# Kernel optimization log

Hardware: AMD Instinct MI355X
Metric: run time of the kernel (lower is better)

## Reference

```python
import jax, jax.numpy as jnp
import numpy as np

D, H, DH, L, DFF, V, K = 512, 8, 64, 6, 2048, 256, 5
N = 10240
TAU = 0.1
EPS = 1e-5


def _ln(x, w, b):
    m = x.mean(-1, keepdims=True)
    v = ((x - m) ** 2).mean(-1, keepdims=True)
    return (x - m) * jax.lax.rsqrt(v + EPS) * w + b


def _attn(q_in, kv_in, inw, inb, ow, ob):
    # q_in: [Q, D], kv_in: [M, D]; standard PyTorch MultiheadAttention math
    wq, wk, wv = jnp.split(inw, 3, 0)
    bq, bk, bv = jnp.split(inb, 3)
    q = (q_in @ wq.T + bq).reshape(-1, H, DH)
    k = (kv_in @ wk.T + bk).reshape(-1, H, DH)
    v = (kv_in @ wv.T + bv).reshape(-1, H, DH)
    s = jnp.einsum('qhd,mhd->hqm', q, k) / np.float32(np.sqrt(DH))
    o = jnp.einsum('hqm,mhd->qhd', jax.nn.softmax(s, -1), v).reshape(-1, D)
    return o @ ow.T + ob


def setup_inputs() -> dict:
    key = jax.random.key(0)
    ks = iter(jax.random.split(key, 64))

    def w(shape):
        return jax.random.normal(next(ks), shape, jnp.float32) * 0.02

    inp = {
        'input_bytes': jax.random.randint(next(ks), (N,), 0, V, jnp.int32),
        'emb': w((V, D)),
        'alpha': jnp.float32(0.5),
        'enc_inw': w((L, 3 * D, D)), 'enc_inb': w((L, 3 * D)),
        'enc_ow': w((L, D, D)), 'enc_ob': w((L, D)),
        'enc_w1': w((L, DFF, D)), 'enc_b1': w((L, DFF)),
        'enc_w2': w((L, D, DFF)), 'enc_b2': w((L, D)),
        'enc_ln1w': jnp.ones((L, D)), 'enc_ln1b': jnp.zeros((L, D)),
        'enc_ln2w': jnp.ones((L, D)), 'enc_ln2b': jnp.zeros((L, D)),
        'dec_sa_inw': w((L, 3 * D, D)), 'dec_sa_inb': w((L, 3 * D)),
        'dec_sa_ow': w((L, D, D)), 'dec_sa_ob': w((L, D)),
        'dec_ca_inw': w((L, 3 * D, D)), 'dec_ca_inb': w((L, 3 * D)),
        'dec_ca_ow': w((L, D, D)), 'dec_ca_ob': w((L, D)),
        'dec_w1': w((L, DFF, D)), 'dec_b1': w((L, DFF)),
        'dec_w2': w((L, D, DFF)), 'dec_b2': w((L, D)),
        'dec_ln1w': jnp.ones((L, D)), 'dec_ln1b': jnp.zeros((L, D)),
        'dec_ln2w': jnp.ones((L, D)), 'dec_ln2b': jnp.zeros((L, D)),
        'dec_ln3w': jnp.ones((L, D)), 'dec_ln3b': jnp.zeros((L, D)),
        'out_w': w((V, D)), 'out_b': w((V,)),
    }
    return inp


def reference(input_bytes, emb, alpha, enc_inw, enc_inb, enc_ow, enc_ob,
              enc_w1, enc_b1, enc_w2, enc_b2, enc_ln1w, enc_ln1b, enc_ln2w, enc_ln2b,
              dec_sa_inw, dec_sa_inb, dec_sa_ow, dec_sa_ob,
              dec_ca_inw, dec_ca_inb, dec_ca_ow, dec_ca_ob,
              dec_w1, dec_b1, dec_w2, dec_b2,
              dec_ln1w, dec_ln1b, dec_ln2w, dec_ln2b, dec_ln3w, dec_ln3b,
              out_w, out_b):
    P = input_bytes.shape[0] // K
    patches = input_bytes[:P * K].reshape(P, K)            # fixed k-byte patching
    x = emb[patches].mean(1)                               # mean-pooled patch embeddings [P, D]
    # ---- TransformerEncoder (post-LN, relu FFN, no dropout at eval) ----
    for l in range(L):
        x = _ln(x + _attn(x, x, enc_inw[l], enc_inb[l], enc_ow[l], enc_ob[l]), enc_ln1w[l], enc_ln1b[l])
        ff = jax.nn.relu(x @ enc_w1[l].T + enc_b1[l]) @ enc_w2[l].T + enc_b2[l]
        x = _ln(x + ff, enc_ln2w[l], enc_ln2b[l])
    encoded = x                                            # [P, D]
    # ---- gating + embedding mix (vectorized over the per-patch loop) ----
    gate = jnp.linalg.norm(encoded, axis=-1) > TAU
    tok = emb[patches[:, -1]]
    x = jnp.where(gate[:, None], alpha * encoded + (1.0 - alpha) * tok, tok)  # [P, D]
    # ---- TransformerDecoder: each patch is an independent length-1 target;
    #      self-attn over a single token reduces to out_proj(V(x));
    #      cross-attn attends to the full encoded memory (as in the original loop) ----
    for l in range(L):
        wv = dec_sa_inw[l][2 * D:]
        bv = dec_sa_inb[l][2 * D:]
        sa = (x @ wv.T + bv) @ dec_sa_ow[l].T + dec_sa_ob[l]
        x = _ln(x + sa, dec_ln1w[l], dec_ln1b[l])
        ca = _attn(x, encoded, dec_ca_inw[l], dec_ca_inb[l], dec_ca_ow[l], dec_ca_ob[l])
        x = _ln(x + ca, dec_ln2w[l], dec_ln2b[l])
        ff = jax.nn.relu(x @ dec_w1[l].T + dec_b1[l]) @ dec_w2[l].T + dec_b2[l]
        x = _ln(x + ff, dec_ln3w[l], dec_ln3b[l])
    return x @ out_w.T + out_b                             # [P, V]
```

## Files before the change

### kernel.cpp

```cpp
#include <hip/hip_runtime.h>
#include <hip/hip_bf16.h>
#include <math.h>

#define DD   512
#define HN   8
#define DHD  64
#define LL   6
#define DFF_ 2048
#define VV   256
#define KB_  5
#define PP   2048
#define EPS_ 1e-5f
#define TAU_ 0.1f
#define NS   4
#define KVS  (PP / NS)

typedef __attribute__((ext_vector_type(8))) short bf16x8;
typedef __attribute__((ext_vector_type(4))) short bf16x4;
typedef __attribute__((ext_vector_type(4))) float f32x4;

__device__ __forceinline__ float wave_sum(float v) {
#pragma unroll
  for (int m = 32; m >= 1; m >>= 1) v += __shfl_xor(v, m, 64);
  return v;
}

__device__ __forceinline__ unsigned short f2bf(float f) {
  unsigned u = __float_as_uint(f);
  u += 0x7FFF + ((u >> 16) & 1);
  return (unsigned short)(u >> 16);
}

__device__ __forceinline__ float bf2f(unsigned short u) {
  return __uint_as_float(((unsigned)u) << 16);
}

__device__ __forceinline__ bf16x8 cvt8(float4 a, float4 b) {
  bf16x8 v;
  v[0] = (short)f2bf(a.x); v[1] = (short)f2bf(a.y);
  v[2] = (short)f2bf(a.z); v[3] = (short)f2bf(a.w);
  v[4] = (short)f2bf(b.x); v[5] = (short)f2bf(b.y);
  v[6] = (short)f2bf(b.z); v[7] = (short)f2bf(b.w);
  return v;
}

__device__ __forceinline__ void gload16(const void* g, void* l) {
  __builtin_amdgcn_global_load_lds(
      (const __attribute__((address_space(1))) unsigned int*)g,
      (__attribute__((address_space(3))) unsigned int*)l, 16, 0, 0);
}

#define NSEG 55
struct CvtSeg { const float* src; short* dst; int n; };
struct CvtArgs { CvtSeg seg[NSEG]; };

__global__ __launch_bounds__(256) void convert_bf16_kernel(CvtArgs a) {
  const CvtSeg sg = a.seg[blockIdx.y];
  const int i = ((int)blockIdx.x * 256 + (int)threadIdx.x) * 16;
  if (i >= sg.n) return;
  const float4 x0 = *(const float4*)(sg.src + i);
  const float4 x1 = *(const float4*)(sg.src + i + 4);
  const float4 x2 = *(const float4*)(sg.src + i + 8);
  const float4 x3 = *(const float4*)(sg.src + i + 12);
  *(bf16x8*)(sg.dst + i)     = cvt8(x0, x1);
  *(bf16x8*)(sg.dst + i + 8) = cvt8(x2, x3);
}

__global__ __launch_bounds__(256) void transpose_wv_kernel(const float* __restrict__ sa_inw,
                                                           short* __restrict__ wvt) {
  __shared__ float t[64][65];
  const int l = blockIdx.z;
  const float* S = sa_inw + (size_t)l * 3 * DD * DD + (size_t)2 * DD * DD;
  short* D = wvt + (size_t)l * DD * DD;
  const int bo = blockIdx.y * 64;
  const int bi = blockIdx.x * 64;
  const int r = (int)threadIdx.x >> 2;
  const int c0 = ((int)threadIdx.x & 3) * 16;
#pragma unroll
  for (int j = 0; j < 16; j += 4)
    *(float4*)&t[r][c0 + j] = *(const float4*)&S[(size_t)(bo + r) * DD + bi + c0 + j];
  __syncthreads();
  bf16x8 o0, o1;
#pragma unroll
  for (int j = 0; j < 8; ++j) o0[j] = (short)f2bf(t[c0 + j][r]);
#pragma unroll
  for (int j = 0; j < 8; ++j) o1[j] = (short)f2bf(t[c0 + 8 + j][r]);
  short* dp = &D[(size_t)(bi + r) * DD + bo + c0];
  *(bf16x8*)dp = o0;
  *(bf16x8*)(dp + 8) = o1;
}

__global__ __launch_bounds__(256) void sa_bias_kernel(const float* __restrict__ sa_inb,
                                                      const float* __restrict__ sa_ow,
                                                      const float* __restrict__ sa_ob,
                                                      float* __restrict__ bc) {
  const int gid = (int)blockIdx.x * 4 + ((int)threadIdx.x >> 6);
  const int l = gid >> 9, n = gid & 511;
  const int lane = (int)threadIdx.x & 63;
  const float* wo = sa_ow + (size_t)l * DD * DD + (size_t)n * DD + lane * 8;
  const float* bv = sa_inb + (size_t)l * 3 * DD + 2 * DD + lane * 8;
  float s = 0.f;
#pragma unroll
  for (int j = 0; j < 8; ++j) s += wo[j] * bv[j];
  s = wave_sum(s);
  if (lane == 0) bc[(size_t)l * DD + n] = s + sa_ob[(size_t)l * DD + n];
}

__global__ __launch_bounds__(256) void gemm_wc_kernel(const short* __restrict__ WoBase,
                                                      size_t astr,
                                                      const short* __restrict__ WvT,
                                                      short* __restrict__ Wc) {
  constexpr int BK = 64;
  __shared__ short As[64 * BK];
  __shared__ short Bs[64 * BK];
  const int l = blockIdx.z;
  const short* A = WoBase + (size_t)l * astr;
  const short* W = WvT + (size_t)l * DD * DD;
  short* C = Wc + (size_t)l * DD * DD;
  const int tid = (int)threadIdx.x;
  const int lane = tid & 63;
  const int wid = tid >> 6;
  const int wm = (wid >> 1) * 32;
  const int wn = (wid & 1) * 32;
  const int bm = blockIdx.y * 64;
  const int bn = blockIdx.x * 64;
  const int fr = lane & 15;
  const int kq = lane >> 4;
  const int rs = fr & 7;
  const int srow = lane >> 3;
  const int scg = (lane & 7) ^ srow;

  f32x4 acc[2][2];
#pragma unroll
  for (int i = 0; i < 2; ++i)
#pragma unroll
    for (int j = 0; j < 2; ++j) acc[i][j] = (f32x4){0.f, 0.f, 0.f, 0.f};

  for (int k0 = 0; k0 < DD; k0 += BK) {
    __syncthreads();
#pragma unroll
    for (int is = 0; is < 2; ++is) {
      const int ib = is * 4 + wid;
      gload16(&A[(size_t)(bm + ib * 8 + srow) * DD + k0 + scg * 8], &As[ib * 512]);
      gload16(&W[(size_t)(bn + ib * 8 + srow) * DD + k0 + scg * 8], &Bs[ib * 512]);
    }
    __syncthreads();
#pragma unroll
    for (int s = 0; s < 2; ++s) {
      const int cg = s * 4 + kq;
      const int co = (cg ^ rs) * 8;
      bf16x8 af[2], bf[2];
#pragma unroll
      for (int i = 0; i < 2; ++i) af[i] = *(const bf16x8*)&As[(wm + i * 16 + fr) * BK + co];
#pragma unroll
      for (int j = 0; j < 2; ++j) bf[j] = *(const bf16x8*)&Bs[(wn + j * 16 + fr) * BK + co];
#pragma unroll
      for (int i = 0; i < 2; ++i)
#pragma unroll
        for (int j = 0; j < 2; ++j)
          acc[i][j] = __builtin_amdgcn_mfma_f32_16x16x32_bf16(af[i], bf[j], acc[i][j], 0, 0, 0);
    }
  }
  const int cr = (lane >> 4) * 4;
#pragma unroll
  for (int j = 0; j < 2; ++j) {
    const int col = bn + wn + j * 16 + fr;
#pragma unroll
    for (int i = 0; i < 2; ++i)
#pragma unroll
      for (int r = 0; r < 4; ++r)
        C[(size_t)(bm + wm + i * 16 + cr + r) * DD + col] = (short)f2bf(acc[i][j][r]);
  }
}

__global__ __launch_bounds__(256) void embed_mean_kernel(const int* __restrict__ bytes,
                                                         const float* __restrict__ emb,
                                                         float* __restrict__ x,
                                                         short* __restrict__ xb,
                                                         float* __restrict__ tok) {
  const int p = blockIdx.x;
  const int d = threadIdx.x * 2;
  float a0 = 0.f, a1 = 0.f;
  int last = 0;
#pragma unroll
  for (int k = 0; k < KB_; ++k) {
    const int idx = bytes[p * KB_ + k];
    last = idx;
    const float* e = emb + (size_t)idx * DD + d;
    a0 += e[0]; a1 += e[1];
  }
  a0 *= 0.2f; a1 *= 0.2f;
  x[(size_t)p * DD + d]     = a0;
  x[(size_t)p * DD + d + 1] = a1;
  xb[(size_t)p * DD + d]     = (short)f2bf(a0);
  xb[(size_t)p * DD + d + 1] = (short)f2bf(a1);
  const float* e = emb + (size_t)last * DD + d;
  tok[(size_t)p * DD + d]     = e[0];
  tok[(size_t)p * DD + d + 1] = e[1];
}

template <int BM, int BN, int NSPLIT, int RELU, int WF32, int WBF16, int QS>
__global__ __launch_bounds__(256) void gemm_gl_kernel(
    const short* __restrict__ A, int lda,
    const short* __restrict__ W, int ldw,
    const float* __restrict__ bias,
    float* __restrict__ Cf, short* __restrict__ Cb, int ldc, int Kd,
    size_t pstride) {
  constexpr int BK = 128;
  __shared__ short As[BM * BK];
  __shared__ short Bs[BN * BK];
  constexpr int WM = BM / 2, WN = BN / 2;
  constexpr int MF = WM / 16, NF = WN / 16;
  const int tid = (int)threadIdx.x;
  const int lane = tid & 63;
  const int wid = tid >> 6;
  const int wm = (wid >> 1) * WM;
  const int wn = (wid & 1) * WN;
  const int bm = blockIdx.y * BM;
  const int bn = blockIdx.x * BN;
  const int fr = lane & 15;
  const int kq = lane >> 4;
  const int srow = lane >> 4;
  const int sc16 = lane & 15;

  const int kz = (NSPLIT > 1) ? (int)blockIdx.z : 0;
  const int kbeg = kz * (Kd / NSPLIT);
  const int kend = kbeg + Kd / NSPLIT;

  f32x4 acc[MF][NF];
#pragma unroll
  for (int i = 0; i < MF; ++i)
#pragma unroll
    for (int j = 0; j < NF; ++j) acc[i][j] = (f32x4){0.f, 0.f, 0.f, 0.f};

  for (int k0 = kbeg; k0 < kend; k0 += BK) {
    __syncthreads();
#pragma unroll
    for (int is = 0; is < BM / 16; ++is) {
      const int ib = is * 4 + wid;
      const int row = ib * 4 + srow;
      const int cg = sc16 ^ (row & 15);
      gload16(&A[(size_t)(bm + row) * lda + k0 + cg * 8], &As[ib * 512]);
    }
#pragma unroll
    for (int is = 0; is < BN / 16; ++is) {
      const int ib = is * 4 + wid;
      const int row = ib * 4 + srow;
      const int cg = sc16 ^ (row & 15);
      gload16(&W[(size_t)(bn + row) * ldw + k0 + cg * 8], &Bs[ib * 512]);
    }
    __syncthreads();
#pragma unroll
    for (int s = 0; s < 4; ++s) {
      const int co = ((s * 4 + kq) ^ fr) * 8;
      bf16x8 af[MF], bf[NF];
#pragma unroll
      for (int i = 0; i < MF; ++i)
        af[i] = *(const bf16x8*)&As[(wm + i * 16 + fr) * BK + co];
#pragma unroll
      for (int j = 0; j < NF; ++j)
        bf[j] = *(const bf16x8*)&Bs[(wn + j * 16 + fr) * BK + co];
#pragma unroll
      for (int i = 0; i < MF; ++i)
#pragma unroll
        for (int j = 0; j < NF; ++j)
          acc[i][j] = __builtin_amdgcn_mfma_f32_16x16x32_bf16(af[i], bf[j], acc[i][j], 0, 0, 0);
    }
  }

  const int cr = (lane >> 4) * 4;
  if constexpr (NSPLIT > 1) {
#pragma unroll
    for (int j = 0; j < NF; ++j) {
      const int col = bn + wn + j * 16 + fr;
#pragma unroll
      for (int i = 0; i < MF; ++i)
#pragma unroll
        for (int r = 0; r < 4; ++r) {
          const size_t idx = (size_t)(bm + wm + i * 16 + cr + r) * ldc + col;
          if (WF32) Cf[(size_t)kz * pstride + idx] = acc[i][j][r];
          else      Cb[(size_t)kz * pstride + idx] = (short)f2bf(acc[i][j][r]);
        }
    }
  } else {
#pragma unroll
    for (int j = 0; j < NF; ++j) {
      const int col = bn + wn + j * 16 + fr;
      const float bb = bias[col];
      const float sc = (QS && col < DD) ? 0.125f : 1.f;
#pragma unroll
      for (int i = 0; i < MF; ++i) {
#pragma unroll
        for (int r = 0; r < 4; ++r) {
          float v = (acc[i][j][r] + bb) * sc;
          if (RELU) v = fmaxf(v, 0.f);
          const size_t idx = (size_t)(bm + wm + i * 16 + cr + r) * ldc + col;
          if (WF32) Cf[idx] = v;
          if (WBF16) Cb[idx] = (short)f2bf(v);
        }
      }
    }
  }
}

__global__ __launch_bounds__(256) void gemm_ca_kernel(
    const short* __restrict__ Aq, const short* __restrict__ Akv,
    const short* __restrict__ Wfull, const float* __restrict__ bias,
    short* __restrict__ Cb) {
  constexpr int BK = 64;
  __shared__ short As[64 * BK];
  __shared__ short Bs[64 * BK];
  const int bx = (int)blockIdx.x;
  const int part_kv = bx >= 8;
  const short* A = part_kv ? Akv : Aq;
  const int wrow0 = part_kv ? DD + (bx - 8) * 64 : bx * 64;
  const float sc = part_kv ? 1.f : 0.125f;
  const int tid = (int)threadIdx.x;
  const int lane = tid & 63;
  const int wid = tid >> 6;
  const int wm = (wid >> 1) * 32;
  const int wn = (wid & 1) * 32;
  const int bm = blockIdx.y * 64;
  const int fr = lane & 15;
  const int kq = lane >> 4;
  const int rs = fr & 7;
  const int srow = lane >> 3;
  const int scg = (lane & 7) ^ srow;

  f32x4 acc[2][2];
#pragma unroll
  for (int i = 0; i < 2; ++i)
#pragma unroll
    for (int j = 0; j < 2; ++j) acc[i][j] = (f32x4){0.f, 0.f, 0.f, 0.f};

  for (int k0 = 0; k0 < DD; k0 += BK) {
    __syncthreads();
#pragma unroll
    for (int is = 0; is < 2; ++is) {
      const int ib = is * 4 + wid;
      gload16(&A[(size_t)(bm + ib * 8 + srow) * DD + k0 + scg * 8], &As[ib * 512]);
      gload16(&Wfull[(size_t)(wrow0 + ib * 8 + srow) * DD + k0 + scg * 8], &Bs[ib * 512]);
    }
    __syncthreads();
#pragma unroll
    for (int s = 0; s < 2; ++s) {
      const int cg = s * 4 + kq;
      const int co = (cg ^ rs) * 8;
      bf16x8 af[2], bf[2];
#pragma unroll
      for (int i = 0; i < 2; ++i) af[i] = *(const bf16x8*)&As[(wm + i * 16 + fr) * BK + co];
#pragma unroll
      for (int j = 0; j < 2; ++j) bf[j] = *(const bf16x8*)&Bs[(wn + j * 16 + fr) * BK + co];
#pragma unroll
      for (int i = 0; i < 2; ++i)
#pragma unroll
        for (int j = 0; j < 2; ++j)
          acc[i][j] = __builtin_amdgcn_mfma_f32_16x16x32_bf16(af[i], bf[j], acc[i][j], 0, 0, 0);
    }
  }
  const int cr = (lane >> 4) * 4;
#pragma unroll
  for (int j = 0; j < 2; ++j) {
    const int col = wrow0 + wn + j * 16 + fr;
    const float bb = bias[col];
#pragma unroll
    for (int i = 0; i < 2; ++i)
#pragma unroll
      for (int r = 0; r < 4; ++r)
        Cb[(size_t)(bm + wm + i * 16 + cr + r) * (3 * DD) + col] =
            (short)f2bf((acc[i][j][r] + bb) * sc);
  }
}

__global__ __launch_bounds__(256) void flash_attn_mfma_kernel(const short* __restrict__ qkvb,
                                                              short* __restrict__ Opart,
                                                              float* __restrict__ stats) {
  constexpr int LS = 72;
  __shared__ short Ks[64 * 64];
  __shared__ short Vt[64 * LS];
  __shared__ short Ps[64 * LS];
  const int h = blockIdx.y;
  const int q0 = blockIdx.x * 64;
  const int sp = blockIdx.z;
  const int tid = (int)threadIdx.x;
  const int lane = tid & 63;
  const int wid = tid >> 6;
  const int fr = lane & 15;
  const int g = lane >> 4;
  const int kg = g * 8;
  const int rs3 = fr & 7;

  bf16x8 qf[2];
  {
    const short* src = qkvb + (size_t)(q0 + wid * 16 + fr) * (3 * DD) + h * DHD + kg;
    qf[0] = *(const bf16x8*)src;
    qf[1] = *(const bf16x8*)(src + 32);
  }

  f32x4 acc_o[4];
#pragma unroll
  for (int df = 0; df < 4; ++df) acc_o[df] = (f32x4){0.f, 0.f, 0.f, 0.f};
  float mreg = -INFINITY, lsum = 0.f;

  const int srow8 = lane >> 3;
  const int sscg = (lane & 7) ^ srow8;
  const int vk2 = (tid & 31) * 2;
  const int vd8 = (tid >> 5) * 8;

  for (int t = 0; t < KVS / 64; ++t) {
    const int k0 = sp * KVS + t * 64;
    __syncthreads();
    {
#pragma unroll
      for (int p = 0; p < 2; ++p) {
        const int rb = p * 32 + wid * 8;
        gload16(&qkvb[(size_t)(k0 + rb + srow8) * (3 * DD) + DD + h * DHD + sscg * 8],
                &Ks[rb * 64]);
      }
      const short* vbase = qkvb + (size_t)(k0 + vk2) * (3 * DD) + 2 * DD + h * DHD + vd8;
      const bf16x8 v0 = *(const bf16x8*)vbase;
      const bf16x8 v1 = *(const bf16x8*)(vbase + 3 * DD);
#pragma unroll
      for (int j = 0; j < 8; ++j) {
        const unsigned pk = ((unsigned)(unsigned short)v0[j]) |
                            (((unsigned)(unsigned short)v1[j]) << 16);
        *(unsigned*)&Vt[(vd8 + j) * LS + vk2] = pk;
      }
    }
    __syncthreads();

    f32x4 st[4];
#pragma unroll
    for (int nf = 0; nf < 4; ++nf) st[nf] = (f32x4){0.f, 0.f, 0.f, 0.f};
    __builtin_amdgcn_s_setprio(1);
#pragma unroll
    for (int nf = 0; nf < 4; ++nf) {
      const int krow = (nf * 16 + fr) * 64;
      const bf16x8 kf0 = *(const bf16x8*)&Ks[krow + ((g ^ rs3) * 8)];
      const bf16x8 kf1 = *(const bf16x8*)&Ks[krow + (((g + 4) ^ rs3) * 8)];
      st[nf] = __builtin_amdgcn_mfma_f32_16x16x32_bf16(kf0, qf[0], st[nf], 0, 0, 0);
      st[nf] = __builtin_amdgcn_mfma_f32_16x16x32_bf16(kf1, qf[1], st[nf], 0, 0, 0);
    }
    __builtin_amdgcn_s_setprio(0);

    float mx = st[0][0];
#pragma unroll
    for (int nf = 0; nf < 4; ++nf)
#pragma unroll
      for (int i = 0; i < 4; ++i) mx = fmaxf(mx, st[nf][i]);
    mx = fmaxf(mx, __shfl_xor(mx, 16, 64));
    mx = fmaxf(mx, __shfl_xor(mx, 32, 64));
    const float mn = fmaxf(mreg, mx);
    const float corr = __expf(mreg - mn);
    mreg = mn;
    float pv[4][4];
    float sum = 0.f;
#pragma unroll
    for (int nf = 0; nf < 4; ++nf)
#pragma unroll
      for (int i = 0; i < 4; ++i) {
        pv[nf][i] = __expf(st[nf][i] - mn);
        sum += pv[nf][i];
      }
    sum += __shfl_xor(sum, 16, 64);
    sum += __shfl_xor(sum, 32, 64);
    lsum = lsum * corr + sum;

    float corr_acc[4];
#pragma unroll
    for (int i = 0; i < 4; ++i)
      corr_acc[i] = __shfl(corr, (lane & 48) | (g * 4 + i), 64);
#pragma unroll
    for (int df = 0; df < 4; ++df) {
      acc_o[df][0] *= corr_acc[0]; acc_o[df][1] *= corr_acc[1];
      acc_o[df][2] *= corr_acc[2]; acc_o[df][3] *= corr_acc[3];
    }

#pragma unroll
    for (int nf = 0; nf < 4; ++nf) {
      bf16x4 pw;
#pragma unroll
      for (int i = 0; i < 4; ++i) pw[i] = (short)f2bf(pv[nf][i]);
      *(bf16x4*)&Ps[(wid * 16 + fr) * LS + nf * 16 + g * 4] = pw;
    }
    asm volatile("s_waitcnt lgkmcnt(0)" ::: "memory");

    const bf16x8 pa0 = *(const bf16x8*)&Ps[(wid * 16 + fr) * LS + kg];
    const bf16x8 pa1 = *(const bf16x8*)&Ps[(wid * 16 + fr) * LS + kg + 32];
    __builtin_amdgcn_s_setprio(1);
#pragma unroll
    for (int df = 0; df < 4; ++df) {
      const bf16x8 vb0 = *(const bf16x8*)&Vt[(df * 16 + fr) * LS + kg];
      const bf16x8 vb1 = *(const bf16x8*)&Vt[(df * 16 + fr) * LS + kg + 32];
      acc_o[df] = __builtin_amdgcn_mfma_f32_16x16x32_bf16(pa0, vb0, acc_o[df], 0, 0, 0);
      acc_o[df] = __builtin_amdgcn_mfma_f32_16x16x32_bf16(pa1, vb1, acc_o[df], 0, 0, 0);
    }
    __builtin_amdgcn_s_setprio(0);
  }

  const int orow = q0 + wid * 16 + g * 4;
#pragma unroll
  for (int df = 0; df < 4; ++df)
#pragma unroll
    for (int i = 0; i < 4; ++i)
      Opart[((size_t)sp * PP + orow + i) * DD + h * DHD + df * 16 + fr] =
          (short)f2bf(acc_o[df][i]);
  if (g == 0) {
    const size_t si = (((size_t)sp * PP + q0 + wid * 16 + fr) * HN + h) * 2;
    stats[si]     = mreg;
    stats[si + 1] = lsum;
  }
}

__global__ __launch_bounds__(256) void attn_combine_kernel(const short* __restrict__ Opart,
                                                           const float* __restrict__ stats,
                                                           short* __restrict__ outb) {
  const int row = blockIdx.x * 4 + ((int)threadIdx.x >> 6);
  const int lane = (int)threadIdx.x & 63;
  const int d0 = lane * 8;
  const int h = d0 >> 6;
  float m[NS], l[NS];
  float M = -INFINITY;
#pragma unroll
  for (int s = 0; s < NS; ++s) {
    const size_t si = (((size_t)s * PP + row) * HN + h) * 2;
    m[s] = stats[si]; l[s] = stats[si + 1];
    M = fmaxf(M, m[s]);
  }
  float L = 0.f;
  float o[8];
#pragma unroll
  for (int j = 0; j < 8; ++j) o[j] = 0.f;
#pragma unroll
  for (int s = 0; s < NS; ++s) {
    const float e = __expf(m[s] - M);
    L += l[s] * e;
    const bf16x8 v = *(const bf16x8*)&Opart[((size_t)s * PP + row) * DD + d0];
#pragma unroll
    for (int j = 0; j < 8; ++j) o[j] += bf2f((unsigned short)v[j]) * e;
  }
  const float inv = 1.f / L;
  bf16x8 ob;
#pragma unroll
  for (int j = 0; j < 8; ++j) ob[j] = (short)f2bf(o[j] * inv);
  *(bf16x8*)&outb[(size_t)row * DD + d0] = ob;
}

__global__ __launch_bounds__(256) void ln_residual_kernel(const float* __restrict__ xin,
                                                          const short* __restrict__ pA,
                                                          const short* __restrict__ pB,
                                                          const float* __restrict__ gb,
                                                          const float* __restrict__ w,
                                                          const float* __restrict__ b,
                                                          float* __restrict__ out,
                                                          short* __restrict__ outb) {
  const int row = blockIdx.x * 4 + (threadIdx.x >> 6);
  const int lane = threadIdx.x & 63;
  const size_t base = (size_t)row * DD + lane * 8;
  float v[8];
  {
    const float4 a0 = *(const float4*)&xin[base];
    const float4 a1 = *(const float4*)&xin[base + 4];
    const bf16x8 r = *(const bf16x8*)&pA[base];
    const bf16x8 s = *(const bf16x8*)&pB[base];
    const float4 g0 = *(const float4*)&gb[lane * 8];
    const float4 g1 = *(const float4*)&gb[lane * 8 + 4];
    v[0] = a0.x + bf2f((unsigned short)r[0]) + bf2f((unsigned short)s[0]) + g0.x;
    v[1] = a0.y + bf2f((unsigned short)r[1]) + bf2f((unsigned short)s[1]) + g0.y;
    v[2] = a0.z + bf2f((unsigned short)r[2]) + bf2f((unsigned short)s[2]) + g0.z;
    v[3] = a0.w + bf2f((unsigned short)r[3]) + bf2f((unsigned short)s[3]) + g0.w;
    v[4] = a1.x + bf2f((unsigned short)r[4]) + bf2f((unsigned short)s[4]) + g1.x;
    v[5] = a1.y + bf2f((unsigned short)r[5]) + bf2f((unsigned short)s[5]) + g1.y;
    v[6] = a1.z + bf2f((unsigned short)r[6]) + bf2f((unsigned short)s[6]) + g1.z;
    v[7] = a1.w + bf2f((unsigned short)r[7]) + bf2f((unsigned short)s[7]) + g1.w;
  }
  float sum = 0.f;
#pragma unroll
  for (int j = 0; j < 8; ++j) sum += v[j];
  sum = wave_sum(sum);
  const float mean = sum * (1.f / DD);
  float sq = 0.f;
#pragma unroll
  for (int j = 0; j < 8; ++j) { const float dd = v[j] - mean; sq += dd * dd; }
  sq = wave_sum(sq);
  const float rstd = rsqrtf(sq * (1.f / DD) + EPS_);
  const float* wp = w + lane * 8;
  const float* bp = b + lane * 8;
  float o[8];
#pragma unroll
  for (int j = 0; j < 8; ++j) o[j] = (v[j] - mean) * rstd * wp[j] + bp[j];
  *(float4*)&out[base] = *(float4*)&o[0];
  *(float4*)&out[base + 4] = *(float4*)&o[4];
  bf16x8 ob;
#pragma unroll
  for (int j = 0; j < 8; ++j) ob[j] = (short)f2bf(o[j]);
  *(bf16x8*)&outb[base] = ob;
}

__global__ __launch_bounds__(256) void ln_gate_kernel(const float* __restrict__ xin,
                                                      const short* __restrict__ pA,
                                                      const short* __restrict__ pB,
                                                      const float* __restrict__ gb,
                                                      const float* __restrict__ w,
                                                      const float* __restrict__ b,
                                                      const float* __restrict__ tok,
                                                      const float* __restrict__ alpha_p,
                                                      float* __restrict__ xout,
                                                      short* __restrict__ xb,
                                                      short* __restrict__ encb) {
  const int row = blockIdx.x * 4 + (threadIdx.x >> 6);
  const int lane = threadIdx.x & 63;
  const size_t base = (size_t)row * DD + lane * 8;
  float v[8];
  {
    const float4 a0 = *(const float4*)&xin[base];
    const float4 a1 = *(const float4*)&xin[base + 4];
    const bf16x8 r = *(const bf16x8*)&pA[base];
    const bf16x8 s = *(const bf16x8*)&pB[base];
    const float4 g0 = *(const float4*)&gb[lane * 8];
    const float4 g1 = *(const float4*)&gb[lane * 8 + 4];
    v[0] = a0.x + bf2f((unsigned short)r[0]) + bf2f((unsigned short)s[0]) + g0.x;
    v[1] = a0.y + bf2f((unsigned short)r[1]) + bf2f((unsigned short)s[1]) + g0.y;
    v[2] = a0.z + bf2f((unsigned short)r[2]) + bf2f((unsigned short)s[2]) + g0.z;
    v[3] = a0.w + bf2f((unsigned short)r[3]) + bf2f((unsigned short)s[3]) + g0.w;
    v[4] = a1.x + bf2f((unsigned short)r[4]) + bf2f((unsigned short)s[4]) + g1.x;
    v[5] = a1.y + bf2f((unsigned short)r[5]) + bf2f((unsigned short)s[5]) + g1.y;
    v[6] = a1.z + bf2f((unsigned short)r[6]) + bf2f((unsigned short)s[6]) + g1.z;
    v[7] = a1.w + bf2f((unsigned short)r[7]) + bf2f((unsigned short)s[7]) + g1.w;
  }
  float sum = 0.f;
#pragma unroll
  for (int j = 0; j < 8; ++j) sum += v[j];
  sum = wave_sum(sum);
  const float mean = sum * (1.f / DD);
  float sq = 0.f;
#pragma unroll
  for (int j = 0; j < 8; ++j) { const float dd = v[j] - mean; sq += dd * dd; }
  sq = wave_sum(sq);
  const float rstd = rsqrtf(sq * (1.f / DD) + EPS_);
  const float* wp = w + lane * 8;
  const float* bp = b + lane * 8;
  float e[8];
#pragma unroll
  for (int j = 0; j < 8; ++j) e[j] = (v[j] - mean) * rstd * wp[j] + bp[j];
  bf16x8 eb;
#pragma unroll
  for (int j = 0; j < 8; ++j) eb[j] = (short)f2bf(e[j]);
  *(bf16x8*)&encb[base] = eb;
  float nsq = 0.f;
#pragma unroll
  for (int j = 0; j < 8; ++j) nsq += e[j] * e[j];
  nsq = wave_sum(nsq);
  const bool gate = nsq > TAU_ * TAU_;
  const float a = *alpha_p;
  float t[8];
  {
    const float4 b0 = *(const float4*)&tok[base];
    const float4 b1 = *(const float4*)&tok[base + 4];
    t[0] = b0.x; t[1] = b0.y; t[2] = b0.z; t[3] = b0.w;
    t[4] = b1.x; t[5] = b1.y; t[6] = b1.z; t[7] = b1.w;
  }
  float o[8];
#pragma unroll
  for (int j = 0; j < 8; ++j) o[j] = gate ? (a * e[j] + (1.f - a) * t[j]) : t[j];
  *(float4*)&xout[base] = *(float4*)&o[0];
  *(float4*)&xout[base + 4] = *(float4*)&o[4];
  bf16x8 ob;
#pragma unroll
  for (int j = 0; j < 8; ++j) ob[j] = (short)f2bf(o[j]);
  *(bf16x8*)&xb[base] = ob;
}

__global__ __launch_bounds__(256) void out_combine_kernel(const float* __restrict__ P0,
                                                          const float* __restrict__ P1,
                                                          const float* __restrict__ bias,
                                                          float* __restrict__ out) {
  const size_t i = ((size_t)blockIdx.x * 256 + threadIdx.x) * 4;
  const int col = (int)(i % VV);
  const float4 a = *(const float4*)&P0[i];
  const float4 b = *(const float4*)&P1[i];
  const float4 c = *(const float4*)&bias[col];
  float4 o;
  o.x = a.x + b.x + c.x; o.y = a.y + b.y + c.y;
  o.z = a.z + b.z + c.z; o.w = a.w + b.w + c.w;
  *(float4*)&out[i] = o;
}

extern "C" void kernel_launch(void* const* d_in, const int* in_sizes, int n_in,
                              void* d_out, int out_size, void* d_ws, size_t ws_size,
                              hipStream_t stream) {
  const int*   bytes    = (const int*)d_in[0];
  const float* emb      = (const float*)d_in[1];
  const float* alpha    = (const float*)d_in[2];
  const float* enc_inw  = (const float*)d_in[3];
  const float* enc_inb  = (const float*)d_in[4];
  const float* enc_ow   = (const float*)d_in[5];
  const float* enc_ob   = (const float*)d_in[6];
  const float* enc_w1   = (const float*)d_in[7];
  const float* enc_b1   = (const float*)d_in[8];
  const float* enc_w2   = (const float*)d_in[9];
  const float* enc_b2   = (const float*)d_in[10];
  const float* enc_ln1w = (const float*)d_in[11];
  const float* enc_ln1b = (const float*)d_in[12];
  const float* enc_ln2w = (const float*)d_in[13];
  const float* enc_ln2b = (const float*)d_in[14];
  const float* dec_sa_inw = (const float*)d_in[15];
  const float* dec_sa_inb = (const float*)d_in[16];
  const float* dec_sa_ow  = (const float*)d_in[17];
  const float* dec_sa_ob  = (const float*)d_in[18];
  const float* dec_ca_inw = (const float*)d_in[19];
  const float* dec_ca_inb = (const float*)d_in[20];
  const float* dec_ca_ow  = (const float*)d_in[21];
  const float* dec_ca_ob  = (const float*)d_in[22];
  const float* dec_w1   = (const float*)d_in[23];
  const float* dec_b1   = (const float*)d_in[24];
  const float* dec_w2   = (const float*)d_in[25];
  const float* dec_b2   = (const float*)d_in[26];
  const float* dec_ln1w = (const float*)d_in[27];
  const float* dec_ln1b = (const float*)d_in[28];
  const float* dec_ln2w = (const float*)d_in[29];
  const float* dec_ln2b = (const float*)d_in[30];
  const float* dec_ln3w = (const float*)d_in[31];
  const float* dec_ln3b = (const float*)d_in[32];
  const float* out_w    = (const float*)d_in[33];
  const float* out_b    = (const float*)d_in[34];

  float* fp = (float*)d_ws;
  float* x     = fp;  fp += (size_t)PP * DD;
  float* tok   = fp;  fp += (size_t)PP * DD;
  float* stats = fp;  fp += (size_t)NS * PP * HN * 2;
  float* outP  = fp;  fp += (size_t)2 * PP * VV;
  float* bcbuf = fp;  fp += (size_t)LL * DD;
  short* sp = (short*)fp;
  short* OpartB  = sp;  sp += (size_t)NS * PP * DD;
  short* tmpB    = sp;  sp += (size_t)2 * PP * DD;
  short* x_bf    = sp;  sp += (size_t)PP * DD;
  short* enc_bf  = sp;  sp += (size_t)PP * DD;
  short* qkv_bf  = sp;  sp += (size_t)PP * 3 * DD;
  short* attno_bf= sp;  sp += (size_t)PP * DD;
  short* ffh_bf  = sp;  sp += (size_t)PP * DFF_;
  short* wvT     = sp;  sp += (size_t)LL * DD * DD;
  short* wcM     = sp;  sp += (size_t)LL * DD * DD;
  short* warena  = sp;

  CvtArgs ca;
  size_t eoff[LL][4], doff[LL][5], ooff;
  size_t dec_start = 0, dec_stride = 0;
  {
    int si = 0;
    size_t off = 0;
    const size_t n0 = 3 * DD * DD, n1 = DD * DD, n2 = (size_t)DFF_ * DD, n3 = (size_t)DD * DFF_;
    for (int l = 0; l < LL; ++l) {
      ca.seg[si++] = {enc_inw + (size_t)l * n0, warena + off, (int)n0}; eoff[l][0] = off; off += n0;
      ca.seg[si++] = {enc_ow  + (size_t)l * n1, warena + off, (int)n1}; eoff[l][1] = off; off += n1;
      ca.seg[si++] = {enc_w1  + (size_t)l * n2, warena + off, (int)n2}; eoff[l][2] = off; off += n2;
      ca.seg[si++] = {enc_w2  + (size_t)l * n3, warena + off, (int)n3}; eoff[l][3] = off; off += n3;
    }
    dec_start = off;
    for (int l = 0; l < LL; ++l) {
      const size_t o0 = off;
      ca.seg[si++] = {dec_sa_ow  + (size_t)l * n1, warena + off, (int)n1}; doff[l][0] = off; off += n1;
      ca.seg[si++] = {dec_ca_inw + (size_t)l * n0, warena + off, (int)n0}; doff[l][1] = off; off += n0;
      ca.seg[si++] = {dec_ca_ow  + (size_t)l * n1, warena + off, (int)n1}; doff[l][2] = off; off += n1;
      ca.seg[si++] = {dec_w1     + (size_t)l * n2, warena + off, (int)n2}; doff[l][3] = off; off += n2;
      ca.seg[si++] = {dec_w2     + (size_t)l * n3, warena + off, (int)n3}; doff[l][4] = off; off += n3;
      if (l == 0) dec_stride = off - o0; (void)o0;
    }
    ca.seg[si++] = {out_w, warena + off, VV * DD}; ooff = off;
  }

  const dim3 b256(256);
  const dim3 gFA(PP / 64, HN, NS);
  const dim3 gQKV(3 * DD / 64, PP / 128);
  const dim3 gFF1(DFF_ / 64, PP / 128);
  const dim3 gS(DD / 64, PP / 64, 2);
  const dim3 gCA(24, PP / 64);
  const dim3 gOUTg(VV / 64, PP / 64, 2);
  const size_t psD = (size_t)PP * DD;
  const size_t psV = (size_t)PP * VV;

  convert_bf16_kernel<<<dim3(256, NSEG), b256, 0, stream>>>(ca);
  transpose_wv_kernel<<<dim3(8, 8, LL), b256, 0, stream>>>(dec_sa_inw, wvT);
  sa_bias_kernel<<<(LL * DD) / 4, b256, 0, stream>>>(dec_sa_inb, dec_sa_ow, dec_sa_ob, bcbuf);
  gemm_wc_kernel<<<dim3(8, 8, LL), b256, 0, stream>>>(warena + dec_start, dec_stride, wvT, wcM);
  embed_mean_kernel<<<PP, b256, 0, stream>>>(bytes, emb, x, x_bf, tok);

  for (int l = 0; l < LL; ++l) {
    const float* inb = enc_inb + (size_t)l * 3 * DD;
    const float* ob  = enc_ob  + (size_t)l * DD;
    const float* b1  = enc_b1  + (size_t)l * DFF_;
    const float* b2  = enc_b2  + (size_t)l * DD;

    gemm_gl_kernel<128, 64, 1, 0, 0, 1, 1><<<gQKV, b256, 0, stream>>>(
        x_bf, DD, warena + eoff[l][0], DD, inb, nullptr, qkv_bf, 3 * DD, DD, 0);
    flash_attn_mfma_kernel<<<gFA, b256, 0, stream>>>(qkv_bf, OpartB, stats);
    attn_combine_kernel<<<PP / 4, b256, 0, stream>>>(OpartB, stats, attno_bf);
    gemm_gl_kernel<64, 64, 2, 0, 0, 0, 0><<<gS, b256, 0, stream>>>(
        attno_bf, DD, warena + eoff[l][1], DD, nullptr, nullptr, tmpB, DD, DD, psD);
    ln_residual_kernel<<<PP / 4, b256, 0, stream>>>(
        x, tmpB, tmpB + psD, ob, enc_ln1w + (size_t)l * DD, enc_ln1b + (size_t)l * DD, x, x_bf);
    gemm_gl_kernel<128, 64, 1, 1, 0, 1, 0><<<gFF1, b256, 0, stream>>>(
        x_bf, DD, warena + eoff[l][2], DD, b1, nullptr, ffh_bf, DFF_, DD, 0);
    gemm_gl_kernel<64, 64, 2, 0, 0, 0, 0><<<gS, b256, 0, stream>>>(
        ffh_bf, DFF_, warena + eoff[l][3], DFF_, nullptr, nullptr, tmpB, DD, DFF_, psD);
    if (l + 1 < LL) {
      ln_residual_kernel<<<PP / 4, b256, 0, stream>>>(
          x, tmpB, tmpB + psD, b2, enc_ln2w + (size_t)l * DD, enc_ln2b + (size_t)l * DD, x, x_bf);
    } else {
      ln_gate_kernel<<<PP / 4, b256, 0, stream>>>(
          x, tmpB, tmpB + psD, b2, enc_ln2w + (size_t)l * DD, enc_ln2b + (size_t)l * DD,
          tok, alpha, x, x_bf, enc_bf);
    }
  }

  for (int l = 0; l < LL; ++l) {
    const float* ca_inb = dec_ca_inb + (size_t)l * 3 * DD;
    const float* ca_ob  = dec_ca_ob + (size_t)l * DD;
    const float* b1 = dec_b1 + (size_t)l * DFF_;
    const float* b2 = dec_b2 + (size_t)l * DD;

    gemm_gl_kernel<64, 64, 2, 0, 0, 0, 0><<<gS, b256, 0, stream>>>(
        x_bf, DD, wcM + (size_t)l * DD * DD, DD, nullptr, nullptr, tmpB, DD, DD, psD);
    ln_residual_kernel<<<PP / 4, b256, 0, stream>>>(
        x, tmpB, tmpB + psD, bcbuf + (size_t)l * DD,
        dec_ln1w + (size_t)l * DD, dec_ln1b + (size_t)l * DD, x, x_bf);

    gemm_ca_kernel<<<gCA, b256, 0, stream>>>(
        x_bf, enc_bf, warena + doff[l][1], ca_inb, qkv_bf);
    flash_attn_mfma_kernel<<<gFA, b256, 0, stream>>>(qkv_bf, OpartB, stats);
    attn_combine_kernel<<<PP / 4, b256, 0, stream>>>(OpartB, stats, attno_bf);
    gemm_gl_kernel<64, 64, 2, 0, 0, 0, 0><<<gS, b256, 0, stream>>>(
        attno_bf, DD, warena + doff[l][2], DD, nullptr, nullptr, tmpB, DD, DD, psD);
    ln_residual_kernel<<<PP / 4, b256, 0, stream>>>(
        x, tmpB, tmpB + psD, ca_ob, dec_ln2w + (size_t)l * DD, dec_ln2b + (size_t)l * DD, x, x_bf);

    gemm_gl_kernel<128, 64, 1, 1, 0, 1, 0><<<gFF1, b256, 0, stream>>>(
        x_bf, DD, warena + doff[l][3], DD, b1, nullptr, ffh_bf, DFF_, DD, 0);
    gemm_gl_kernel<64, 64, 2, 0, 0, 0, 0><<<gS, b256, 0, stream>>>(
        ffh_bf, DFF_, warena + doff[l][4], DFF_, nullptr, nullptr, tmpB, DD, DFF_, psD);
    ln_residual_kernel<<<PP / 4, b256, 0, stream>>>(
        x, tmpB, tmpB + psD, b2, dec_ln3w + (size_t)l * DD, dec_ln3b + (size_t)l * DD, x, x_bf);
  }

  gemm_gl_kernel<64, 64, 2, 0, 1, 0, 0><<<gOUTg, b256, 0, stream>>>(
      x_bf, DD, warena + ooff, DD, nullptr, outP, nullptr, VV, DD, psV);
  out_combine_kernel<<<(PP * VV / 4) / 256, b256, 0, stream>>>(
      outP, outP + psV, out_b, (float*)d_out);
}
```

Measured before the change: 989.8 us.

## Drop fp32 residual stream, use exp2 softmax with lazy max rescaling

The fp32 copy of the residual stream is removed, so the layernorm kernels read and write only the bf16 activation buffer. The flash-attention softmax moves to base-2 exponentials by folding log2(e) into the query scale. It also skips the running-max rescale of the accumulators unless the new maximum exceeds the old one by a threshold. This cuts memory traffic in the LN kernels and exp/shuffle work in attention, at the cost of keeping the residual stream only in bf16 across all layers.

After: 981.4 us. About the same (-0.8%).

```diff
diff --git a/kernel.cpp b/kernel.cpp
--- a/kernel.cpp
+++ b/kernel.cpp
@@ -14,6 +14,8 @@
 #define TAU_ 0.1f
 #define NS   4
 #define KVS  (PP / NS)
+#define QSCALE 0.18033688f
+#define THRL2  11.5416f
 
 typedef __attribute__((ext_vector_type(8))) short bf16x8;
 typedef __attribute__((ext_vector_type(4))) short bf16x4;
@@ -175,7 +177,6 @@
 
 __global__ __launch_bounds__(256) void embed_mean_kernel(const int* __restrict__ bytes,
                                                          const float* __restrict__ emb,
-                                                         float* __restrict__ x,
                                                          short* __restrict__ xb,
                                                          float* __restrict__ tok) {
   const int p = blockIdx.x;
@@ -189,11 +190,8 @@
     const float* e = emb + (size_t)idx * DD + d;
     a0 += e[0]; a1 += e[1];
   }
-  a0 *= 0.2f; a1 *= 0.2f;
-  x[(size_t)p * DD + d]     = a0;
-  x[(size_t)p * DD + d + 1] = a1;
-  xb[(size_t)p * DD + d]     = (short)f2bf(a0);
-  xb[(size_t)p * DD + d + 1] = (short)f2bf(a1);
+  xb[(size_t)p * DD + d]     = (short)f2bf(a0 * 0.2f);
+  xb[(size_t)p * DD + d + 1] = (short)f2bf(a1 * 0.2f);
   const float* e = emb + (size_t)last * DD + d;
   tok[(size_t)p * DD + d]     = e[0];
   tok[(size_t)p * DD + d + 1] = e[1];
@@ -287,7 +285,7 @@
     for (int j = 0; j < NF; ++j) {
       const int col = bn + wn + j * 16 + fr;
       const float bb = bias[col];
-      const float sc = (QS && col < DD) ? 0.125f : 1.f;
+      const float sc = (QS && col < DD) ? QSCALE : 1.f;
 #pragma unroll
       for (int i = 0; i < MF; ++i) {
 #pragma unroll
@@ -314,7 +312,7 @@
   const int part_kv = bx >= 8;
   const short* A = part_kv ? Akv : Aq;
   const int wrow0 = part_kv ? DD + (bx - 8) * 64 : bx * 64;
-  const float sc = part_kv ? 1.f : 0.125f;
+  const float sc = part_kv ? 1.f : QSCALE;
   const int tid = (int)threadIdx.x;
   const int lane = tid & 63;
   const int wid = tid >> 6;
@@ -450,31 +448,35 @@
       for (int i = 0; i < 4; ++i) mx = fmaxf(mx, st[nf][i]);
     mx = fmaxf(mx, __shfl_xor(mx, 16, 64));
     mx = fmaxf(mx, __shfl_xor(mx, 32, 64));
-    const float mn = fmaxf(mreg, mx);
-    const float corr = __expf(mreg - mn);
-    mreg = mn;
+
+    if (!__all(mx <= mreg + THRL2)) {
+      const float mn = fmaxf(mreg, mx);
+      const float corr = exp2f(mreg - mn);
+      mreg = mn;
+      lsum *= corr;
+      float corr_acc[4];
+#pragma unroll
+      for (int i = 0; i < 4; ++i)
+        corr_acc[i] = __shfl(corr, (lane & 48) | (g * 4 + i), 64);
+#pragma unroll
+      for (int df = 0; df < 4; ++df) {
+        acc_o[df][0] *= corr_acc[0]; acc_o[df][1] *= corr_acc[1];
+        acc_o[df][2] *= corr_acc[2]; acc_o[df][3] *= corr_acc[3];
+      }
+    }
+
     float pv[4][4];
     float sum = 0.f;
 #pragma unroll
     for (int nf = 0; nf < 4; ++nf)
 #pragma unroll
       for (int i = 0; i < 4; ++i) {
-        pv[nf][i] = __expf(st[nf][i] - mn);
+        pv[nf][i] = exp2f(st[nf][i] - mreg);
         sum += pv[nf][i];
       }
     sum += __shfl_xor(sum, 16, 64);
     sum += __shfl_xor(sum, 32, 64);
-    lsum = lsum * corr + sum;
-
-    float corr_acc[4];
-#pragma unroll
-    for (int i = 0; i < 4; ++i)
-      corr_acc[i] = __shfl(corr, (lane & 48) | (g * 4 + i), 64);
-#pragma unroll
-    for (int df = 0; df < 4; ++df) {
-      acc_o[df][0] *= corr_acc[0]; acc_o[df][1] *= corr_acc[1];
-      acc_o[df][2] *= corr_acc[2]; acc_o[df][3] *= corr_acc[3];
-    }
+    lsum += sum;
 
 #pragma unroll
     for (int nf = 0; nf < 4; ++nf) {
@@ -533,7 +535,7 @@
   for (int j = 0; j < 8; ++j) o[j] = 0.f;
 #pragma unroll
   for (int s = 0; s < NS; ++s) {
-    const float e = __expf(m[s] - M);
+    const float e = exp2f(m[s] - M);
     L += l[s] * e;
     const bf16x8 v = *(const bf16x8*)&Opart[((size_t)s * PP + row) * DD + d0];
 #pragma unroll
@@ -546,33 +548,28 @@
   *(bf16x8*)&outb[(size_t)row * DD + d0] = ob;
 }
 
-__global__ __launch_bounds__(256) void ln_residual_kernel(const float* __restrict__ xin,
+__global__ __launch_bounds__(256) void ln_residual_kernel(const short* __restrict__ xin,
                                                           const short* __restrict__ pA,
                                                           const short* __restrict__ pB,
                                                           const float* __restrict__ gb,
                                                           const float* __restrict__ w,
                                                           const float* __restrict__ b,
-                                                          float* __restrict__ out,
                                                           short* __restrict__ outb) {
   const int row = blockIdx.x * 4 + (threadIdx.x >> 6);
   const int lane = threadIdx.x & 63;
   const size_t base = (size_t)row * DD + lane * 8;
   float v[8];
   {
-    const float4 a0 = *(const float4*)&xin[base];
-    const float4 a1 = *(const float4*)&xin[base + 4];
+    const bf16x8 a = *(const bf16x8*)&xin[base];
     const bf16x8 r = *(const bf16x8*)&pA[base];
     const bf16x8 s = *(const bf16x8*)&pB[base];
     const float4 g0 = *(const float4*)&gb[lane * 8];
     const float4 g1 = *(const float4*)&gb[lane * 8 + 4];
-    v[0] = a0.x + bf2f((unsigned short)r[0]) + bf2f((unsigned short)s[0]) + g0.x;
-    v[1] = a0.y + bf2f((unsigned short)r[1]) + bf2f((unsigned short)s[1]) + g0.y;
-    v[2] = a0.z + bf2f((unsigned short)r[2]) + bf2f((unsigned short)s[2]) + g0.z;
-    v[3] = a0.w + bf2f((unsigned short)r[3]) + bf2f((unsigned short)s[3]) + g0.w;
-    v[4] = a1.x + bf2f((unsigned short)r[4]) + bf2f((unsigned short)s[4]) + g1.x;
-    v[5] = a1.y + bf2f((unsigned short)r[5]) + bf2f((unsigned short)s[5]) + g1.y;
-    v[6] = a1.z + bf2f((unsigned short)r[6]) + bf2f((unsigned short)s[6]) + g1.z;
-    v[7] = a1.w + bf2f((unsigned short)r[7]) + bf2f((unsigned short)s[7]) + g1.w;
+    const float gg[8] = {g0.x, g0.y, g0.z, g0.w, g1.x, g1.y, g1.z, g1.w};
+#pragma unroll
+    for (int j = 0; j < 8; ++j)
+      v[j] = bf2f((unsigned short)a[j]) + bf2f((unsigned short)r[j]) +
+             bf2f((unsigned short)s[j]) + gg[j];
   }
   float sum = 0.f;
 #pragma unroll
@@ -586,18 +583,14 @@
   const float rstd = rsqrtf(sq * (1.f / DD) + EPS_);
   const float* wp = w + lane * 8;
   const float* bp = b + lane * 8;
-  float o[8];
-#pragma unroll
-  for (int j = 0; j < 8; ++j) o[j] = (v[j] - mean) * rstd * wp[j] + bp[j];
-  *(float4*)&out[base] = *(float4*)&o[0];
-  *(float4*)&out[base + 4] = *(float4*)&o[4];
   bf16x8 ob;
 #pragma unroll
-  for (int j = 0; j < 8; ++j) ob[j] = (short)f2bf(o[j]);
+  for (int j = 0; j < 8; ++j)
+    ob[j] = (short)f2bf((v[j] - mean) * rstd * wp[j] + bp[j]);
   *(bf16x8*)&outb[base] = ob;
 }
 
-__global__ __launch_bounds__(256) void ln_gate_kernel(const float* __restrict__ xin,
+__global__ __launch_bounds__(256) void ln_gate_kernel(const short* __restrict__ xin,
                                                       const short* __restrict__ pA,
                                                       const short* __restrict__ pB,
                                                       const float* __restrict__ gb,
@@ -605,7 +598,6 @@
                                                       const float* __restrict__ b,
                                                       const float* __restrict__ tok,
                                                       const float* __restrict__ alpha_p,
-                                                      float* __restrict__ xout,
                                                       short* __restrict__ xb,
                                                       short* __restrict__ encb) {
   const int row = blockIdx.x * 4 + (threadIdx.x >> 6);
@@ -613,20 +605,16 @@
   const size_t base = (size_t)row * DD + lane * 8;
   float v[8];
   {
-    const float4 a0 = *(const float4*)&xin[base];
-    const float4 a1 = *(const float4*)&xin[base + 4];
+    const bf16x8 a = *(const bf16x8*)&xin[base];
     const bf16x8 r = *(const bf16x8*)&pA[base];
     const bf16x8 s = *(const bf16x8*)&pB[base];
     const float4 g0 = *(const float4*)&gb[lane * 8];
     const float4 g1 = *(const float4*)&gb[lane * 8 + 4];
-    v[0] = a0.x + bf2f((unsigned short)r[0]) + bf2f((unsigned short)s[0]) + g0.x;
-    v[1] = a0.y + bf2f((unsigned short)r[1]) + bf2f((unsigned short)s[1]) + g0.y;
-    v[2] = a0.z + bf2f((unsigned short)r[2]) + bf2f((unsigned short)s[2]) + g0.z;
-    v[3] = a0.w + bf2f((unsigned short)r[3]) + bf2f((unsigned short)s[3]) + g0.w;
-    v[4] = a1.x + bf2f((unsigned short)r[4]) + bf2f((unsigned short)s[4]) + g1.x;
-    v[5] = a1.y + bf2f((unsigned short)r[5]) + bf2f((unsigned short)s[5]) + g1.y;
-    v[6] = a1.z + bf2f((unsigned short)r[6]) + bf2f((unsigned short)s[6]) + g1.z;
-    v[7] = a1.w + bf2f((unsigned short)r[7]) + bf2f((unsigned short)s[7]) + g1.w;
+    const float gg[8] = {g0.x, g0.y, g0.z, g0.w, g1.x, g1.y, g1.z, g1.w};
+#pragma unroll
+    for (int j = 0; j < 8; ++j)
+      v[j] = bf2f((unsigned short)a[j]) + bf2f((unsigned short)r[j]) +
+             bf2f((unsigned short)s[j]) + gg[j];
   }
   float sum = 0.f;
 #pragma unroll
@@ -660,14 +648,10 @@
     t[0] = b0.x; t[1] = b0.y; t[2] = b0.z; t[3] = b0.w;
     t[4] = b1.x; t[5] = b1.y; t[6] = b1.z; t[7] = b1.w;
   }
-  float o[8];
-#pragma unroll
-  for (int j = 0; j < 8; ++j) o[j] = gate ? (a * e[j] + (1.f - a) * t[j]) : t[j];
-  *(float4*)&xout[base] = *(float4*)&o[0];
-  *(float4*)&xout[base + 4] = *(float4*)&o[4];
   bf16x8 ob;
 #pragma unroll
-  for (int j = 0; j < 8; ++j) ob[j] = (short)f2bf(o[j]);
+  for (int j = 0; j < 8; ++j)
+    ob[j] = (short)f2bf(gate ? (a * e[j] + (1.f - a) * t[j]) : t[j]);
   *(bf16x8*)&xb[base] = ob;
 }
 
@@ -726,7 +710,6 @@
   const float* out_b    = (const float*)d_in[34];
 
   float* fp = (float*)d_ws;
-  float* x     = fp;  fp += (size_t)PP * DD;
   float* tok   = fp;  fp += (size_t)PP * DD;
   float* stats = fp;  fp += (size_t)NS * PP * HN * 2;
   float* outP  = fp;  fp += (size_t)2 * PP * VV;
@@ -783,7 +766,7 @@
   transpose_wv_kernel<<<dim3(8, 8, LL), b256, 0, stream>>>(dec_sa_inw, wvT);
   sa_bias_kernel<<<(LL * DD) / 4, b256, 0, stream>>>(dec_sa_inb, dec_sa_ow, dec_sa_ob, bcbuf);
   gemm_wc_kernel<<<dim3(8, 8, LL), b256, 0, stream>>>(warena + dec_start, dec_stride, wvT, wcM);
-  embed_mean_kernel<<<PP, b256, 0, stream>>>(bytes, emb, x, x_bf, tok);
+  embed_mean_kernel<<<PP, b256, 0, stream>>>(bytes, emb, x_bf, tok);
 
   for (int l = 0; l < LL; ++l) {
     const float* inb = enc_inb + (size_t)l * 3 * DD;
@@ -798,18 +781,18 @@
     gemm_gl_kernel<64, 64, 2, 0, 0, 0, 0><<<gS, b256, 0, stream>>>(
         attno_bf, DD, warena + eoff[l][1], DD, nullptr, nullptr, tmpB, DD, DD, psD);
     ln_residual_kernel<<<PP / 4, b256, 0, stream>>>(
-        x, tmpB, tmpB + psD, ob, enc_ln1w + (size_t)l * DD, enc_ln1b + (size_t)l * DD, x, x_bf);
+        x_bf, tmpB, tmpB + psD, ob, enc_ln1w + (size_t)l * DD, enc_ln1b + (size_t)l * DD, x_bf);
     gemm_gl_kernel<128, 64, 1, 1, 0, 1, 0><<<gFF1, b256, 0, stream>>>(
         x_bf, DD, warena + eoff[l][2], DD, b1, nullptr, ffh_bf, DFF_, DD, 0);
     gemm_gl_kernel<64, 64, 2, 0, 0, 0, 0><<<gS, b256, 0, stream>>>(
         ffh_bf, DFF_, warena + eoff[l][3], DFF_, nullptr, nullptr, tmpB, DD, DFF_, psD);
     if (l + 1 < LL) {
       ln_residual_kernel<<<PP / 4, b256, 0, stream>>>(
-          x, tmpB, tmpB + psD, b2, enc_ln2w + (size_t)l * DD, enc_ln2b + (size_t)l * DD, x, x_bf);
+          x_bf, tmpB, tmpB + psD, b2, enc_ln2w + (size_t)l * DD, enc_ln2b + (size_t)l * DD, x_bf);
     } else {
       ln_gate_kernel<<<PP / 4, b256, 0, stream>>>(
-          x, tmpB, tmpB + psD, b2, enc_ln2w + (size_t)l * DD, enc_ln2b + (size_t)l * DD,
-          tok, alpha, x, x_bf, enc_bf);
+          x_bf, tmpB, tmpB + psD, b2, enc_ln2w + (size_t)l * DD, enc_ln2b + (size_t)l * DD,
+          tok, alpha, x_bf, enc_bf);
     }
   }
 
@@ -822,8 +805,8 @@
     gemm_gl_kernel<64, 64, 2, 0, 0, 0, 0><<<gS, b256, 0, stream>>>(
         x_bf, DD, wcM + (size_t)l * DD * DD, DD, nullptr, nullptr, tmpB, DD, DD, psD);
     ln_residual_kernel<<<PP / 4, b256, 0, stream>>>(
-        x, tmpB, tmpB + psD, bcbuf + (size_t)l * DD,
-        dec_ln1w + (size_t)l * DD, dec_ln1b + (size_t)l * DD, x, x_bf);
+        x_bf, tmpB, tmpB + psD, bcbuf + (size_t)l * DD,
+        dec_ln1w + (size_t)l * DD, dec_ln1b + (size_t)l * DD, x_bf);
 
     gemm_ca_kernel<<<gCA, b256, 0, stream>>>(
         x_bf, enc_bf, warena + doff[l][1], ca_inb, qkv_bf);
@@ -832,14 +815,14 @@
     gemm_gl_kernel<64, 64, 2, 0, 0, 0, 0><<<gS, b256, 0, stream>>>(
         attno_bf, DD, warena + doff[l][2], DD, nullptr, nullptr, tmpB, DD, DD, psD);
     ln_residual_kernel<<<PP / 4, b256, 0, stream>>>(
-        x, tmpB, tmpB + psD, ca_ob, dec_ln2w + (size_t)l * DD, dec_ln2b + (size_t)l * DD, x, x_bf);
+        x_bf, tmpB, tmpB + psD, ca_ob, dec_ln2w + (size_t)l * DD, dec_ln2b + (size_t)l * DD, x_bf);
 
     gemm_gl_kernel<128, 64, 1, 1, 0, 1, 0><<<gFF1, b256, 0, stream>>>(
         x_bf, DD, warena + doff[l][3], DD, b1, nullptr, ffh_bf, DFF_, DD, 0);
     gemm_gl_kernel<64, 64, 2, 0, 0, 0, 0><<<gS, b256, 0, stream>>>(
         ffh_bf, DFF_, warena + doff[l][4], DFF_, nullptr, nullptr, tmpB, DD, DFF_, psD);
     ln_residual_kernel<<<PP / 4, b256, 0, stream>>>(
-        x, tmpB, tmpB + psD, b2, dec_ln3w + (size_t)l * DD, dec_ln3b + (size_t)l * DD, x, x_bf);
+        x_bf, tmpB, tmpB + psD, b2, dec_ln3w + (size_t)l * DD, dec_ln3b + (size_t)l * DD, x_bf);
   }
 
   gemm_gl_kernel<64, 64, 2, 0, 1, 0, 0><<<gOUTg, b256, 0, stream>>>(
```
